# Kernel tuning notes

Measured on AMD Instinct MI355X. Metric: run time of the kernel, lower is better.

## Reference

```python
import jax, jax.numpy as jnp
import numpy as np

N_EXPERTS = 64
N_ACTIVE = 2
EPS = 1e-8


def setup_inputs() -> dict:
    key = jax.random.key(0)
    k1, k2 = jax.random.split(key)
    x = jax.random.normal(k1, (4, 4096, 2048), dtype=jnp.float32)
    # nn.Linear(dim, n_experts, bias=False) weight: (n_experts, dim)
    W_gate = jax.random.normal(k2, (N_EXPERTS, 2048), dtype=jnp.float32) * (1.0 / np.sqrt(2048))
    return {"x": x, "W_gate": W_gate}


def reference(x, W_gate):
    batch, seq_len, dim = x.shape
    x_flat = x.reshape(-1, dim)                      # (n_tokens, dim)
    n_tokens = x_flat.shape[0]

    logits = jnp.einsum('td,ed->te', x_flat, W_gate)  # (n_tokens, n_experts)
    router_probs = jax.nn.softmax(logits, axis=-1)

    top_k_weights, top_k_indices = jax.lax.top_k(router_probs, N_ACTIVE)
    top_k_weights = top_k_weights / (top_k_weights.sum(axis=-1, keepdims=True) + EPS)

    # Load-balance loss: f_i = fraction of tokens routed to expert i, P_i = mean prob
    one_hot = jax.nn.one_hot(top_k_indices, N_EXPERTS, dtype=jnp.float32)  # (t, k, e)
    tokens_per_expert = one_hot.sum(axis=(0, 1))      # (n_experts,)
    f = tokens_per_expert / (n_tokens * N_ACTIVE)
    P = router_probs.mean(axis=0)
    aux_loss = N_EXPERTS * jnp.sum(f * P)

    return top_k_indices, top_k_weights, aux_loss
```

## Files before the change

### kernel.cpp

```cpp
#include <hip/hip_runtime.h>
#include <math.h>

#define DIM   2048
#define NEXP  64
#define TPB   512
#define TOKB  64
#define KSQ   16

typedef float f32x4  __attribute__((ext_vector_type(4)));
typedef short bf16x8 __attribute__((ext_vector_type(8)));
typedef unsigned short u16;

#define MFMA __builtin_amdgcn_mfma_f32_16x16x32_bf16

__device__ __forceinline__ u16 rne_bf16(float f) {
    union { float f; unsigned u; } v; v.f = f;
    unsigned u = v.u;
    u += 0x7fffu + ((u >> 16) & 1u);
    return (u16)(u >> 16);
}
__device__ __forceinline__ float bf2f(u16 h) {
    union { unsigned u; float f; } v; v.u = ((unsigned)h) << 16;
    return v.f;
}
__device__ __forceinline__ void split3(float x, u16& a, u16& b, u16& c) {
    a = rne_bf16(x);
    float r1 = x - bf2f(a);
    b = rne_bf16(r1);
    float r2 = r1 - bf2f(b);
    c = rne_bf16(r2);
}

__device__ __forceinline__ unsigned cvt_pk(float lo, float hi) {
    unsigned r;
    asm("v_cvt_pk_bf16_f32 %0, %1, %2" : "=v"(r) : "v"(lo), "v"(hi));
    return r;
}
__device__ __forceinline__ float lof(unsigned u) {
    union { unsigned u; float f; } v; v.u = u << 16;
    return v.f;
}
__device__ __forceinline__ float hif(unsigned u) {
    union { unsigned u; float f; } v; v.u = u & 0xffff0000u;
    return v.f;
}

__device__ __forceinline__ void split3x8(f32x4 lo, f32x4 hi,
                                         bf16x8* A0, bf16x8* A1, bf16x8* A2) {
    unsigned w0[4], w1[4], w2[4];
    float e0[4] = {lo.x, lo.z, hi.x, hi.z};
    float e1[4] = {lo.y, lo.w, hi.y, hi.w};
#pragma unroll
    for (int j = 0; j < 4; ++j) {
        float a = e0[j], b = e1[j];
        unsigned p0 = cvt_pk(a, b);
        float r0 = a - lof(p0), r1 = b - hif(p0);
        unsigned p1 = cvt_pk(r0, r1);
        float s0 = r0 - lof(p1), s1 = r1 - hif(p1);
        w0[j] = p0; w1[j] = p1; w2[j] = cvt_pk(s0, s1);
    }
    *A0 = *(bf16x8*)w0;
    *A1 = *(bf16x8*)w1;
    *A2 = *(bf16x8*)w2;
}

#define GLD(GP, LP) __builtin_amdgcn_global_load_lds(                          \
        (const __attribute__((address_space(1))) unsigned*)(GP),               \
        (__attribute__((address_space(3))) unsigned*)(LP), 16, 0, 0)

__global__ __launch_bounds__(256)
void wconv(const float* __restrict__ Wg, u16* __restrict__ wp) {
    const int G  = blockIdx.x * 256 + threadIdx.x;
    const int l  = G & 63;
    const int r  = G >> 6;
    const int ks = r >> 2, et = r & 3;
    const int ex = et * 16 + (l & 15);
    const int k  = ks * 32 + (l >> 4) * 8;
    const float* src = Wg + (size_t)ex * DIM + k;
    f32x4 v0 = *(const f32x4*)src;
    f32x4 v1 = *(const f32x4*)(src + 4);
    u16 h0[8], h1[8], h2[8];
#pragma unroll
    for (int i = 0; i < 8; ++i) {
        float xv = (i < 4) ? v0[i] : v1[i - 4];
        split3(xv, h0[i], h1[i], h2[i]);
    }
    u16* dst = wp + ((size_t)(ks * 12 + et * 3)) * 512 + l * 8;
    *(bf16x8*)(dst)        = *(bf16x8*)h0;
    *(bf16x8*)(dst + 512)  = *(bf16x8*)h1;
    *(bf16x8*)(dst + 1024) = *(bf16x8*)h2;
}

__global__ __launch_bounds__(TPB, 2)
void router_main(const float* __restrict__ x, const u16* __restrict__ wp,
                 float* __restrict__ out, float* __restrict__ gCnt,
                 float* __restrict__ gPsum, int n_tokens) {
    __shared__ __align__(16) unsigned char smem[4 * 2 * 12 * 1024];
    __shared__ float cnt[NEXP];
    __shared__ float rs[TOKB];
    u16 (*bq)[2][12][512] = (u16 (*)[2][12][512])smem;
    float (*ls)[TOKB][68] = (float (*)[TOKB][68])smem;

    const int tid  = threadIdx.x;
    const int lane = tid & 63;
    const int wid  = tid >> 6;
    const int ttg  = wid & 1;
    const int kq   = wid >> 1;
    const int t0   = blockIdx.x * TOKB;

    if (tid < NEXP) cnt[tid] = 0.f;

    f32x4 acc[2][4];
#pragma unroll
    for (int t2 = 0; t2 < 2; ++t2)
#pragma unroll
        for (int et = 0; et < 4; ++et) acc[t2][et] = (f32x4){0.f, 0.f, 0.f, 0.f};

    const float* xs0 = x + (size_t)(t0 + 32 * ttg + (lane & 15)) * DIM
                         + kq * (KSQ * 32) + 8 * (lane >> 4);
    const float* xs1 = xs0 + (size_t)16 * DIM;

#define STAGEB(C) do {                                                         \
        const int g_ = kq * KSQ + (C);                                         \
        const u16* gp_ = wp + ((size_t)g_ * 12 + 6 * ttg) * 512 + lane * 8;    \
        _Pragma("unroll")                                                      \
        for (int f = 0; f < 6; ++f)                                            \
            GLD(gp_ + (size_t)f * 512, &bq[kq][(C) & 1][6 * ttg + f][0]);      \
    } while (0)

#define LOADX(S0, S1, S2, S3, C) do {                                          \
        S0 = *(const f32x4*)(xs0 + (C) * 32);                                  \
        S1 = *(const f32x4*)(xs0 + (C) * 32 + 4);                              \
        S2 = *(const f32x4*)(xs1 + (C) * 32);                                  \
        S3 = *(const f32x4*)(xs1 + (C) * 32 + 4);                              \
    } while (0)

#define ITER(C, S0, S1, S2, S3) do {                                           \
        if ((C) + 1 < KSQ) STAGEB((C) + 1);                                    \
        bf16x8 A00, A01, A02, A10, A11, A12;                                   \
        split3x8(S0, S1, &A00, &A01, &A02);                                    \
        split3x8(S2, S3, &A10, &A11, &A12);                                    \
        if ((C) + 2 < KSQ) LOADX(S0, S1, S2, S3, (C) + 2);                     \
        _Pragma("unroll")                                                      \
        for (int et = 0; et < 4; ++et) {                                       \
            bf16x8 B0 = *(const bf16x8*)&bq[kq][(C) & 1][et * 3 + 0][lane * 8];\
            bf16x8 B1 = *(const bf16x8*)&bq[kq][(C) & 1][et * 3 + 1][lane * 8];\
            bf16x8 B2 = *(const bf16x8*)&bq[kq][(C) & 1][et * 3 + 2][lane * 8];\
            acc[0][et] = MFMA(A00, B0, acc[0][et], 0, 0, 0);                   \
            acc[0][et] = MFMA(A00, B1, acc[0][et], 0, 0, 0);                   \
            acc[0][et] = MFMA(A01, B0, acc[0][et], 0, 0, 0);                   \
            acc[0][et] = MFMA(A01, B1, acc[0][et], 0, 0, 0);                   \
            acc[0][et] = MFMA(A00, B2, acc[0][et], 0, 0, 0);                   \
            acc[0][et] = MFMA(A02, B0, acc[0][et], 0, 0, 0);                   \
            acc[1][et] = MFMA(A10, B0, acc[1][et], 0, 0, 0);                   \
            acc[1][et] = MFMA(A10, B1, acc[1][et], 0, 0, 0);                   \
            acc[1][et] = MFMA(A11, B0, acc[1][et], 0, 0, 0);                   \
            acc[1][et] = MFMA(A11, B1, acc[1][et], 0, 0, 0);                   \
            acc[1][et] = MFMA(A10, B2, acc[1][et], 0, 0, 0);                   \
            acc[1][et] = MFMA(A12, B0, acc[1][et], 0, 0, 0);                   \
        }                                                                      \
        __syncthreads();                                                       \
    } while (0)

    f32x4 pa0, pa1, pa2, pa3, pb0, pb1, pb2, pb3;
    STAGEB(0);
    LOADX(pa0, pa1, pa2, pa3, 0);
    LOADX(pb0, pb1, pb2, pb3, 1);
    __syncthreads();

    for (int cc = 0; cc < KSQ; cc += 2) {
        ITER(cc,     pa0, pa1, pa2, pa3);
        ITER(cc + 1, pb0, pb1, pb2, pb3);
    }
#undef ITER
#undef LOADX
#undef STAGEB

    {
        const int e0 = lane & 15;
#pragma unroll
        for (int t2 = 0; t2 < 2; ++t2) {
            const int mr = 32 * ttg + 16 * t2 + 4 * (lane >> 4);
#pragma unroll
            for (int r = 0; r < 4; ++r) {
                ls[kq][mr + r][e0]      = acc[t2][0][r];
                ls[kq][mr + r][e0 + 16] = acc[t2][1][r];
                ls[kq][mr + r][e0 + 32] = acc[t2][2][r];
                ls[kq][mr + r][e0 + 48] = acc[t2][3][r];
            }
        }
    }
    __syncthreads();

#pragma unroll
    for (int r2 = 0; r2 < 2; ++r2) {
        const int idx = tid + TPB * r2;
        const int tk  = idx >> 4;
        const int e4  = (idx & 15) * 4;
        f32x4 v = *(const f32x4*)&ls[0][tk][e4];
        v = v + *(const f32x4*)&ls[1][tk][e4];
        v = v + *(const f32x4*)&ls[2][tk][e4];
        v = v + *(const f32x4*)&ls[3][tk][e4];
        *(f32x4*)&ls[0][tk][e4] = v;
    }
    __syncthreads();

    const int tok = tid >> 3;
    const int sub = tid & 7;
    float l8[8];
#pragma unroll
    for (int j = 0; j < 8; ++j) l8[j] = ls[0][tok][sub * 8 + j];
    float m1 = -1e30f, m2 = -1e30f;
    int   i1 = 0, i2 = 0;
#pragma unroll
    for (int j = 0; j < 8; ++j) {
        float v = l8[j]; int e = sub * 8 + j;
        if (v > m1)      { m2 = m1; i2 = i1; m1 = v; i1 = e; }
        else if (v > m2) { m2 = v; i2 = e; }
    }
#pragma unroll
    for (int off = 1; off < 8; off <<= 1) {
        float n1 = __shfl_xor(m1, off, 8); int j1 = __shfl_xor(i1, off, 8);
        float n2 = __shfl_xor(m2, off, 8); int j2 = __shfl_xor(i2, off, 8);
        bool fb = (m1 > n1) || (m1 == n1 && i1 < j1);
        float a1 = fb ? m1 : n1;  int ai = fb ? i1 : j1;
        float b1 = fb ? n1 : m1;  int bi = fb ? j1 : i1;
        float c2 = fb ? m2 : n2;  int ci = fb ? i2 : j2;
        bool bb = (b1 > c2) || (b1 == c2 && bi < ci);
        m1 = a1; i1 = ai;
        m2 = bb ? b1 : c2; i2 = bb ? bi : ci;
    }
    float psum = 0.f;
#pragma unroll
    for (int j = 0; j < 8; ++j) {
        float p = __expf(l8[j] - m1);
        psum += p;
        ls[0][tok][sub * 8 + j] = p;
    }
#pragma unroll
    for (int off = 1; off < 8; off <<= 1) psum += __shfl_xor(psum, off, 8);
    const float inv = 1.f / psum;
    if (sub == 0) {
        rs[tok] = inv;
        const float p1 = inv;
        const float p2 = __expf(m2 - m1) * inv;
        const float d  = p1 + p2 + 1e-8f;
        const int tg = t0 + tok;
        out[(size_t)tg * 2]     = (float)i1;
        out[(size_t)tg * 2 + 1] = (float)i2;
        out[(size_t)n_tokens * 2 + (size_t)tg * 2]     = p1 / d;
        out[(size_t)n_tokens * 2 + (size_t)tg * 2 + 1] = p2 / d;
        atomicAdd(&cnt[i1], 1.f);
        atomicAdd(&cnt[i2], 1.f);
    }
    __syncthreads();

    if (tid < NEXP) {
        float cs = 0.f;
#pragma unroll 8
        for (int t = 0; t < TOKB; ++t) cs += ls[0][t][tid] * rs[t];
        atomicAdd(&gPsum[tid], cs);
        atomicAdd(&gCnt[tid], cnt[tid]);
    }
}

__global__ void router_aux(const float* __restrict__ gCnt,
                           const float* __restrict__ gPsum,
                           float* __restrict__ out, int n_tokens) {
    const int e = threadIdx.x;
    float f = gCnt[e] / (float)(n_tokens * 2);
    float P = gPsum[e] / (float)n_tokens;
    float v = f * P;
#pragma unroll
    for (int o = 32; o > 0; o >>= 1) v += __shfl_down(v, o);
    if (e == 0) out[(size_t)n_tokens * 4] = 64.f * v;
}

extern "C" void kernel_launch(void* const* d_in, const int* in_sizes, int n_in,
                              void* d_out, int out_size, void* d_ws, size_t ws_size,
                              hipStream_t stream) {
    const float* x  = (const float*)d_in[0];
    const float* Wg = (const float*)d_in[1];
    float* out = (float*)d_out;
    const int n_tokens = in_sizes[0] / DIM;

    u16*   wplanes = (u16*)d_ws;
    float* gCnt    = (float*)((char*)d_ws + 256 * 3 * 512 * sizeof(u16));
    float* gPsum   = gCnt + NEXP;

    hipMemsetAsync(gCnt, 0, 2 * NEXP * sizeof(float), stream);
    hipLaunchKernelGGL(wconv, dim3(64), dim3(256), 0, stream, Wg, wplanes);
    hipLaunchKernelGGL(router_main, dim3(n_tokens / TOKB), dim3(TPB), 0, stream,
                       x, wplanes, out, gCnt, gPsum, n_tokens);
    hipLaunchKernelGGL(router_aux, dim3(1), dim3(NEXP), 0, stream,
                       gCnt, gPsum, out, n_tokens);
}
```

Before: 54.49 us.

## Give each wave private weight buffers and drop per-chunk block barriers

Re-partitions the eight waves from 2 token groups × 4 K-quarters to 2 token groups × 2 expert halves × 2 K-halves. Each wave now stages its own weight slice into a private double buffer, so the per-chunk __syncthreads is replaced by explicit vmcnt/lgkmcnt waits and sched barriers, with prefetch two chunks ahead. The x loads are now duplicated across the two expert-half waves, and the K-split reduction shrinks from four partials to two. The hand-written waitcnt counts depend on how many loads each wave issues, so a wrong count would risk reading a buffer before it has landed.

```diff
diff --git a/kernel.cpp b/kernel.cpp
--- a/kernel.cpp
+++ b/kernel.cpp
@@ -5,7 +5,7 @@
 #define NEXP  64
 #define TPB   512
 #define TOKB  64
-#define KSQ   16
+#define NKS   32
 
 typedef float f32x4  __attribute__((ext_vector_type(4)));
 typedef short bf16x8 __attribute__((ext_vector_type(8)));
@@ -95,37 +95,38 @@
 void router_main(const float* __restrict__ x, const u16* __restrict__ wp,
                  float* __restrict__ out, float* __restrict__ gCnt,
                  float* __restrict__ gPsum, int n_tokens) {
-    __shared__ __align__(16) unsigned char smem[4 * 2 * 12 * 1024];
+    __shared__ __align__(16) unsigned char smem[8 * 2 * 6 * 1024];
     __shared__ float cnt[NEXP];
     __shared__ float rs[TOKB];
-    u16 (*bq)[2][12][512] = (u16 (*)[2][12][512])smem;
+    u16 (*bq)[2][6][512] = (u16 (*)[2][6][512])smem;
     float (*ls)[TOKB][68] = (float (*)[TOKB][68])smem;
 
     const int tid  = threadIdx.x;
     const int lane = tid & 63;
     const int wid  = tid >> 6;
     const int ttg  = wid & 1;
-    const int kq   = wid >> 1;
+    const int eh   = (wid >> 1) & 1;
+    const int kh   = wid >> 2;
     const int t0   = blockIdx.x * TOKB;
 
     if (tid < NEXP) cnt[tid] = 0.f;
 
-    f32x4 acc[2][4];
+    f32x4 acc[2][2];
 #pragma unroll
     for (int t2 = 0; t2 < 2; ++t2)
 #pragma unroll
-        for (int et = 0; et < 4; ++et) acc[t2][et] = (f32x4){0.f, 0.f, 0.f, 0.f};
+        for (int e2 = 0; e2 < 2; ++e2) acc[t2][e2] = (f32x4){0.f, 0.f, 0.f, 0.f};
 
     const float* xs0 = x + (size_t)(t0 + 32 * ttg + (lane & 15)) * DIM
-                         + kq * (KSQ * 32) + 8 * (lane >> 4);
+                         + kh * (NKS * 32) + 8 * (lane >> 4);
     const float* xs1 = xs0 + (size_t)16 * DIM;
 
 #define STAGEB(C) do {                                                         \
-        const int g_ = kq * KSQ + (C);                                         \
-        const u16* gp_ = wp + ((size_t)g_ * 12 + 6 * ttg) * 512 + lane * 8;    \
+        const int g_ = kh * NKS + (C);                                         \
+        const u16* gp_ = wp + ((size_t)g_ * 12 + 6 * eh) * 512 + lane * 8;     \
         _Pragma("unroll")                                                      \
         for (int f = 0; f < 6; ++f)                                            \
-            GLD(gp_ + (size_t)f * 512, &bq[kq][(C) & 1][6 * ttg + f][0]);      \
+            GLD(gp_ + (size_t)f * 512, &bq[wid][(C) & 1][f][0]);               \
     } while (0)
 
 #define LOADX(S0, S1, S2, S3, C) do {                                          \
@@ -136,39 +137,54 @@
     } while (0)
 
 #define ITER(C, S0, S1, S2, S3) do {                                           \
-        if ((C) + 1 < KSQ) STAGEB((C) + 1);                                    \
+        if ((C) + 1 < NKS) asm volatile("s_waitcnt vmcnt(10)" ::: "memory");   \
+        else               asm volatile("s_waitcnt vmcnt(0)"  ::: "memory");   \
+        __builtin_amdgcn_sched_barrier(0);                                     \
+        bf16x8 B00 = *(const bf16x8*)&bq[wid][(C) & 1][0][lane * 8];           \
+        bf16x8 B01 = *(const bf16x8*)&bq[wid][(C) & 1][1][lane * 8];           \
+        bf16x8 B02 = *(const bf16x8*)&bq[wid][(C) & 1][2][lane * 8];           \
+        bf16x8 B10 = *(const bf16x8*)&bq[wid][(C) & 1][3][lane * 8];           \
+        bf16x8 B11 = *(const bf16x8*)&bq[wid][(C) & 1][4][lane * 8];           \
+        bf16x8 B12 = *(const bf16x8*)&bq[wid][(C) & 1][5][lane * 8];           \
         bf16x8 A00, A01, A02, A10, A11, A12;                                   \
         split3x8(S0, S1, &A00, &A01, &A02);                                    \
         split3x8(S2, S3, &A10, &A11, &A12);                                    \
-        if ((C) + 2 < KSQ) LOADX(S0, S1, S2, S3, (C) + 2);                     \
-        _Pragma("unroll")                                                      \
-        for (int et = 0; et < 4; ++et) {                                       \
-            bf16x8 B0 = *(const bf16x8*)&bq[kq][(C) & 1][et * 3 + 0][lane * 8];\
-            bf16x8 B1 = *(const bf16x8*)&bq[kq][(C) & 1][et * 3 + 1][lane * 8];\
-            bf16x8 B2 = *(const bf16x8*)&bq[kq][(C) & 1][et * 3 + 2][lane * 8];\
-            acc[0][et] = MFMA(A00, B0, acc[0][et], 0, 0, 0);                   \
-            acc[0][et] = MFMA(A00, B1, acc[0][et], 0, 0, 0);                   \
-            acc[0][et] = MFMA(A01, B0, acc[0][et], 0, 0, 0);                   \
-            acc[0][et] = MFMA(A01, B1, acc[0][et], 0, 0, 0);                   \
-            acc[0][et] = MFMA(A00, B2, acc[0][et], 0, 0, 0);                   \
-            acc[0][et] = MFMA(A02, B0, acc[0][et], 0, 0, 0);                   \
-            acc[1][et] = MFMA(A10, B0, acc[1][et], 0, 0, 0);                   \
-            acc[1][et] = MFMA(A10, B1, acc[1][et], 0, 0, 0);                   \
-            acc[1][et] = MFMA(A11, B0, acc[1][et], 0, 0, 0);                   \
-            acc[1][et] = MFMA(A11, B1, acc[1][et], 0, 0, 0);                   \
-            acc[1][et] = MFMA(A10, B2, acc[1][et], 0, 0, 0);                   \
-            acc[1][et] = MFMA(A12, B0, acc[1][et], 0, 0, 0);                   \
-        }                                                                      \
-        __syncthreads();                                                       \
+        asm volatile("s_waitcnt lgkmcnt(0)" ::: "memory");                     \
+        __builtin_amdgcn_sched_barrier(0);                                     \
+        if ((C) + 2 < NKS) { STAGEB((C) + 2); LOADX(S0, S1, S2, S3, (C) + 2); }\
+        acc[0][0] = MFMA(A00, B00, acc[0][0], 0, 0, 0);                        \
+        acc[0][0] = MFMA(A00, B01, acc[0][0], 0, 0, 0);                        \
+        acc[0][0] = MFMA(A01, B00, acc[0][0], 0, 0, 0);                        \
+        acc[0][0] = MFMA(A01, B01, acc[0][0], 0, 0, 0);                        \
+        acc[0][0] = MFMA(A00, B02, acc[0][0], 0, 0, 0);                        \
+        acc[0][0] = MFMA(A02, B00, acc[0][0], 0, 0, 0);                        \
+        acc[0][1] = MFMA(A00, B10, acc[0][1], 0, 0, 0);                        \
+        acc[0][1] = MFMA(A00, B11, acc[0][1], 0, 0, 0);                        \
+        acc[0][1] = MFMA(A01, B10, acc[0][1], 0, 0, 0);                        \
+        acc[0][1] = MFMA(A01, B11, acc[0][1], 0, 0, 0);                        \
+        acc[0][1] = MFMA(A00, B12, acc[0][1], 0, 0, 0);                        \
+        acc[0][1] = MFMA(A02, B10, acc[0][1], 0, 0, 0);                        \
+        acc[1][0] = MFMA(A10, B00, acc[1][0], 0, 0, 0);                        \
+        acc[1][0] = MFMA(A10, B01, acc[1][0], 0, 0, 0);                        \
+        acc[1][0] = MFMA(A11, B00, acc[1][0], 0, 0, 0);                        \
+        acc[1][0] = MFMA(A11, B01, acc[1][0], 0, 0, 0);                        \
+        acc[1][0] = MFMA(A10, B02, acc[1][0], 0, 0, 0);                        \
+        acc[1][0] = MFMA(A12, B00, acc[1][0], 0, 0, 0);                        \
+        acc[1][1] = MFMA(A10, B10, acc[1][1], 0, 0, 0);                        \
+        acc[1][1] = MFMA(A10, B11, acc[1][1], 0, 0, 0);                        \
+        acc[1][1] = MFMA(A11, B10, acc[1][1], 0, 0, 0);                        \
+        acc[1][1] = MFMA(A11, B11, acc[1][1], 0, 0, 0);                        \
+        acc[1][1] = MFMA(A10, B12, acc[1][1], 0, 0, 0);                        \
+        acc[1][1] = MFMA(A12, B10, acc[1][1], 0, 0, 0);                        \
     } while (0)
 
     f32x4 pa0, pa1, pa2, pa3, pb0, pb1, pb2, pb3;
     STAGEB(0);
     LOADX(pa0, pa1, pa2, pa3, 0);
+    STAGEB(1);
     LOADX(pb0, pb1, pb2, pb3, 1);
-    __syncthreads();
-
-    for (int cc = 0; cc < KSQ; cc += 2) {
+
+    for (int cc = 0; cc < NKS; cc += 2) {
         ITER(cc,     pa0, pa1, pa2, pa3);
         ITER(cc + 1, pb0, pb1, pb2, pb3);
     }
@@ -176,6 +192,8 @@
 #undef LOADX
 #undef STAGEB
 
+    __syncthreads();
+
     {
         const int e0 = lane & 15;
 #pragma unroll
@@ -183,10 +201,8 @@
             const int mr = 32 * ttg + 16 * t2 + 4 * (lane >> 4);
 #pragma unroll
             for (int r = 0; r < 4; ++r) {
-                ls[kq][mr + r][e0]      = acc[t2][0][r];
-                ls[kq][mr + r][e0 + 16] = acc[t2][1][r];
-                ls[kq][mr + r][e0 + 32] = acc[t2][2][r];
-                ls[kq][mr + r][e0 + 48] = acc[t2][3][r];
+                ls[kh][mr + r][32 * eh + e0]      = acc[t2][0][r];
+                ls[kh][mr + r][32 * eh + 16 + e0] = acc[t2][1][r];
             }
         }
     }
@@ -199,8 +215,6 @@
         const int e4  = (idx & 15) * 4;
         f32x4 v = *(const f32x4*)&ls[0][tk][e4];
         v = v + *(const f32x4*)&ls[1][tk][e4];
-        v = v + *(const f32x4*)&ls[2][tk][e4];
-        v = v + *(const f32x4*)&ls[3][tk][e4];
         *(f32x4*)&ls[0][tk][e4] = v;
     }
     __syncthreads();
```

Result: slower. 62.70 us (+15.1%).

## Use 4-wave blocks with per-wave private K slices and barrier-free pipelining

Applied to the files above, without the earlier changes.

Halves the block to 256 threads, so each wave owns one K-quarter and handles all 64 tokens (4 token tiles) instead of splitting tokens across two waves. Each wave now stages its own B fragments and synchronizes with explicit vmcnt/lgkmcnt waits and sched barriers instead of a __syncthreads per K step. This is meant to remove block-wide barrier stalls and raise MFMA density per wave. In exchange it doubles accumulator and prefetch register use and drops to one block per CU in the launch bounds, so occupancy falls. The epilogue is adapted to 4 threads per token.

```diff
diff --git a/kernel.cpp b/kernel.cpp
--- a/kernel.cpp
+++ b/kernel.cpp
@@ -3,7 +3,7 @@
 
 #define DIM   2048
 #define NEXP  64
-#define TPB   512
+#define TPB   256
 #define TOKB  64
 #define KSQ   16
 
@@ -91,7 +91,7 @@
     *(bf16x8*)(dst + 1024) = *(bf16x8*)h2;
 }
 
-__global__ __launch_bounds__(TPB, 2)
+__global__ __launch_bounds__(TPB, 1)
 void router_main(const float* __restrict__ x, const u16* __restrict__ wp,
                  float* __restrict__ out, float* __restrict__ gCnt,
                  float* __restrict__ gPsum, int n_tokens) {
@@ -103,97 +103,129 @@
 
     const int tid  = threadIdx.x;
     const int lane = tid & 63;
-    const int wid  = tid >> 6;
-    const int ttg  = wid & 1;
-    const int kq   = wid >> 1;
+    const int kq   = tid >> 6;
     const int t0   = blockIdx.x * TOKB;
 
     if (tid < NEXP) cnt[tid] = 0.f;
 
-    f32x4 acc[2][4];
-#pragma unroll
-    for (int t2 = 0; t2 < 2; ++t2)
-#pragma unroll
-        for (int et = 0; et < 4; ++et) acc[t2][et] = (f32x4){0.f, 0.f, 0.f, 0.f};
-
-    const float* xs0 = x + (size_t)(t0 + 32 * ttg + (lane & 15)) * DIM
+    f32x4 acc[4][4];
+#pragma unroll
+    for (int t = 0; t < 4; ++t)
+#pragma unroll
+        for (int e = 0; e < 4; ++e) acc[t][e] = (f32x4){0.f, 0.f, 0.f, 0.f};
+
+    const float* xt0 = x + (size_t)(t0 +  0 + (lane & 15)) * DIM
                          + kq * (KSQ * 32) + 8 * (lane >> 4);
-    const float* xs1 = xs0 + (size_t)16 * DIM;
+    const float* xt1 = xt0 + (size_t)16 * DIM;
+    const float* xt2 = xt0 + (size_t)32 * DIM;
+    const float* xt3 = xt0 + (size_t)48 * DIM;
 
 #define STAGEB(C) do {                                                         \
         const int g_ = kq * KSQ + (C);                                         \
-        const u16* gp_ = wp + ((size_t)g_ * 12 + 6 * ttg) * 512 + lane * 8;    \
+        const u16* gp_ = wp + ((size_t)g_ * 12) * 512 + lane * 8;              \
         _Pragma("unroll")                                                      \
-        for (int f = 0; f < 6; ++f)                                            \
-            GLD(gp_ + (size_t)f * 512, &bq[kq][(C) & 1][6 * ttg + f][0]);      \
+        for (int j = 0; j < 12; ++j)                                           \
+            GLD(gp_ + (size_t)j * 512, &bq[kq][(C) & 1][j][0]);                \
     } while (0)
 
-#define LOADX(S0, S1, S2, S3, C) do {                                          \
-        S0 = *(const f32x4*)(xs0 + (C) * 32);                                  \
-        S1 = *(const f32x4*)(xs0 + (C) * 32 + 4);                              \
-        S2 = *(const f32x4*)(xs1 + (C) * 32);                                  \
-        S3 = *(const f32x4*)(xs1 + (C) * 32 + 4);                              \
+#define LOADX(P0, P1, P2, P3, P4, P5, P6, P7, C) do {                          \
+        P0 = *(const f32x4*)(xt0 + (C) * 32);                                  \
+        P1 = *(const f32x4*)(xt0 + (C) * 32 + 4);                              \
+        P2 = *(const f32x4*)(xt1 + (C) * 32);                                  \
+        P3 = *(const f32x4*)(xt1 + (C) * 32 + 4);                              \
+        P4 = *(const f32x4*)(xt2 + (C) * 32);                                  \
+        P5 = *(const f32x4*)(xt2 + (C) * 32 + 4);                              \
+        P6 = *(const f32x4*)(xt3 + (C) * 32);                                  \
+        P7 = *(const f32x4*)(xt3 + (C) * 32 + 4);                              \
     } while (0)
 
-#define ITER(C, S0, S1, S2, S3) do {                                           \
-        if ((C) + 1 < KSQ) STAGEB((C) + 1);                                    \
-        bf16x8 A00, A01, A02, A10, A11, A12;                                   \
-        split3x8(S0, S1, &A00, &A01, &A02);                                    \
-        split3x8(S2, S3, &A10, &A11, &A12);                                    \
-        if ((C) + 2 < KSQ) LOADX(S0, S1, S2, S3, (C) + 2);                     \
-        _Pragma("unroll")                                                      \
-        for (int et = 0; et < 4; ++et) {                                       \
-            bf16x8 B0 = *(const bf16x8*)&bq[kq][(C) & 1][et * 3 + 0][lane * 8];\
-            bf16x8 B1 = *(const bf16x8*)&bq[kq][(C) & 1][et * 3 + 1][lane * 8];\
-            bf16x8 B2 = *(const bf16x8*)&bq[kq][(C) & 1][et * 3 + 2][lane * 8];\
-            acc[0][et] = MFMA(A00, B0, acc[0][et], 0, 0, 0);                   \
-            acc[0][et] = MFMA(A00, B1, acc[0][et], 0, 0, 0);                   \
-            acc[0][et] = MFMA(A01, B0, acc[0][et], 0, 0, 0);                   \
-            acc[0][et] = MFMA(A01, B1, acc[0][et], 0, 0, 0);                   \
-            acc[0][et] = MFMA(A00, B2, acc[0][et], 0, 0, 0);                   \
-            acc[0][et] = MFMA(A02, B0, acc[0][et], 0, 0, 0);                   \
-            acc[1][et] = MFMA(A10, B0, acc[1][et], 0, 0, 0);                   \
-            acc[1][et] = MFMA(A10, B1, acc[1][et], 0, 0, 0);                   \
-            acc[1][et] = MFMA(A11, B0, acc[1][et], 0, 0, 0);                   \
-            acc[1][et] = MFMA(A11, B1, acc[1][et], 0, 0, 0);                   \
-            acc[1][et] = MFMA(A10, B2, acc[1][et], 0, 0, 0);                   \
-            acc[1][et] = MFMA(A12, B0, acc[1][et], 0, 0, 0);                   \
+#define ETILE(E, C) do {                                                       \
+        bf16x8 B0 = *(const bf16x8*)&bq[kq][(C) & 1][(E) * 3 + 0][lane * 8];   \
+        bf16x8 B1 = *(const bf16x8*)&bq[kq][(C) & 1][(E) * 3 + 1][lane * 8];   \
+        bf16x8 B2 = *(const bf16x8*)&bq[kq][(C) & 1][(E) * 3 + 2][lane * 8];   \
+        acc[0][E] = MFMA(A00, B0, acc[0][E], 0, 0, 0);                         \
+        acc[0][E] = MFMA(A00, B1, acc[0][E], 0, 0, 0);                         \
+        acc[0][E] = MFMA(A01, B0, acc[0][E], 0, 0, 0);                         \
+        acc[0][E] = MFMA(A01, B1, acc[0][E], 0, 0, 0);                         \
+        acc[0][E] = MFMA(A00, B2, acc[0][E], 0, 0, 0);                         \
+        acc[0][E] = MFMA(A02, B0, acc[0][E], 0, 0, 0);                         \
+        acc[1][E] = MFMA(A10, B0, acc[1][E], 0, 0, 0);                         \
+        acc[1][E] = MFMA(A10, B1, acc[1][E], 0, 0, 0);                         \
+        acc[1][E] = MFMA(A11, B0, acc[1][E], 0, 0, 0);                         \
+        acc[1][E] = MFMA(A11, B1, acc[1][E], 0, 0, 0);                         \
+        acc[1][E] = MFMA(A10, B2, acc[1][E], 0, 0, 0);                         \
+        acc[1][E] = MFMA(A12, B0, acc[1][E], 0, 0, 0);                         \
+        acc[2][E] = MFMA(A20, B0, acc[2][E], 0, 0, 0);                         \
+        acc[2][E] = MFMA(A20, B1, acc[2][E], 0, 0, 0);                         \
+        acc[2][E] = MFMA(A21, B0, acc[2][E], 0, 0, 0);                         \
+        acc[2][E] = MFMA(A21, B1, acc[2][E], 0, 0, 0);                         \
+        acc[2][E] = MFMA(A20, B2, acc[2][E], 0, 0, 0);                         \
+        acc[2][E] = MFMA(A22, B0, acc[2][E], 0, 0, 0);                         \
+        acc[3][E] = MFMA(A30, B0, acc[3][E], 0, 0, 0);                         \
+        acc[3][E] = MFMA(A30, B1, acc[3][E], 0, 0, 0);                         \
+        acc[3][E] = MFMA(A31, B0, acc[3][E], 0, 0, 0);                         \
+        acc[3][E] = MFMA(A31, B1, acc[3][E], 0, 0, 0);                         \
+        acc[3][E] = MFMA(A30, B2, acc[3][E], 0, 0, 0);                         \
+        acc[3][E] = MFMA(A32, B0, acc[3][E], 0, 0, 0);                         \
+    } while (0)
+
+#define ITER(C, P0, P1, P2, P3, P4, P5, P6, P7) do {                           \
+        if ((C) + 1 < KSQ) asm volatile("s_waitcnt vmcnt(20)" ::: "memory");   \
+        else               asm volatile("s_waitcnt vmcnt(0)"  ::: "memory");   \
+        __builtin_amdgcn_sched_barrier(0);                                     \
+        bf16x8 A00, A01, A02, A10, A11, A12, A20, A21, A22, A30, A31, A32;     \
+        split3x8(P0, P1, &A00, &A01, &A02);                                    \
+        split3x8(P2, P3, &A10, &A11, &A12);                                    \
+        split3x8(P4, P5, &A20, &A21, &A22);                                    \
+        split3x8(P6, P7, &A30, &A31, &A32);                                    \
+        ETILE(0, C);                                                           \
+        ETILE(1, C);                                                           \
+        ETILE(2, C);                                                           \
+        ETILE(3, C);                                                           \
+        asm volatile("s_waitcnt lgkmcnt(0)" ::: "memory");                     \
+        __builtin_amdgcn_sched_barrier(0);                                     \
+        if ((C) + 2 < KSQ) {                                                   \
+            STAGEB((C) + 2);                                                   \
+            LOADX(P0, P1, P2, P3, P4, P5, P6, P7, (C) + 2);                    \
         }                                                                      \
-        __syncthreads();                                                       \
     } while (0)
 
-    f32x4 pa0, pa1, pa2, pa3, pb0, pb1, pb2, pb3;
+    f32x4 pa0, pa1, pa2, pa3, pa4, pa5, pa6, pa7;
+    f32x4 pb0, pb1, pb2, pb3, pb4, pb5, pb6, pb7;
     STAGEB(0);
-    LOADX(pa0, pa1, pa2, pa3, 0);
-    LOADX(pb0, pb1, pb2, pb3, 1);
-    __syncthreads();
+    LOADX(pa0, pa1, pa2, pa3, pa4, pa5, pa6, pa7, 0);
+    STAGEB(1);
+    LOADX(pb0, pb1, pb2, pb3, pb4, pb5, pb6, pb7, 1);
 
     for (int cc = 0; cc < KSQ; cc += 2) {
-        ITER(cc,     pa0, pa1, pa2, pa3);
-        ITER(cc + 1, pb0, pb1, pb2, pb3);
+        ITER(cc,     pa0, pa1, pa2, pa3, pa4, pa5, pa6, pa7);
+        ITER(cc + 1, pb0, pb1, pb2, pb3, pb4, pb5, pb6, pb7);
     }
 #undef ITER
+#undef ETILE
 #undef LOADX
 #undef STAGEB
 
+    __syncthreads();
+
     {
         const int e0 = lane & 15;
 #pragma unroll
-        for (int t2 = 0; t2 < 2; ++t2) {
-            const int mr = 32 * ttg + 16 * t2 + 4 * (lane >> 4);
+        for (int t = 0; t < 4; ++t) {
+            const int mr = 16 * t + 4 * (lane >> 4);
 #pragma unroll
             for (int r = 0; r < 4; ++r) {
-                ls[kq][mr + r][e0]      = acc[t2][0][r];
-                ls[kq][mr + r][e0 + 16] = acc[t2][1][r];
-                ls[kq][mr + r][e0 + 32] = acc[t2][2][r];
-                ls[kq][mr + r][e0 + 48] = acc[t2][3][r];
+                ls[kq][mr + r][e0]      = acc[t][0][r];
+                ls[kq][mr + r][e0 + 16] = acc[t][1][r];
+                ls[kq][mr + r][e0 + 32] = acc[t][2][r];
+                ls[kq][mr + r][e0 + 48] = acc[t][3][r];
             }
         }
     }
     __syncthreads();
 
 #pragma unroll
-    for (int r2 = 0; r2 < 2; ++r2) {
+    for (int r2 = 0; r2 < 4; ++r2) {
         const int idx = tid + TPB * r2;
         const int tk  = idx >> 4;
         const int e4  = (idx & 15) * 4;
@@ -205,23 +237,23 @@
     }
     __syncthreads();
 
-    const int tok = tid >> 3;
-    const int sub = tid & 7;
-    float l8[8];
-#pragma unroll
-    for (int j = 0; j < 8; ++j) l8[j] = ls[0][tok][sub * 8 + j];
+    const int tok = tid >> 2;
+    const int sub = tid & 3;
+    float l16[16];
+#pragma unroll
+    for (int j = 0; j < 16; ++j) l16[j] = ls[0][tok][sub * 16 + j];
     float m1 = -1e30f, m2 = -1e30f;
     int   i1 = 0, i2 = 0;
 #pragma unroll
-    for (int j = 0; j < 8; ++j) {
-        float v = l8[j]; int e = sub * 8 + j;
+    for (int j = 0; j < 16; ++j) {
+        float v = l16[j]; int e = sub * 16 + j;
         if (v > m1)      { m2 = m1; i2 = i1; m1 = v; i1 = e; }
         else if (v > m2) { m2 = v; i2 = e; }
     }
 #pragma unroll
-    for (int off = 1; off < 8; off <<= 1) {
-        float n1 = __shfl_xor(m1, off, 8); int j1 = __shfl_xor(i1, off, 8);
-        float n2 = __shfl_xor(m2, off, 8); int j2 = __shfl_xor(i2, off, 8);
+    for (int off = 1; off < 4; off <<= 1) {
+        float n1 = __shfl_xor(m1, off, 4); int j1 = __shfl_xor(i1, off, 4);
+        float n2 = __shfl_xor(m2, off, 4); int j2 = __shfl_xor(i2, off, 4);
         bool fb = (m1 > n1) || (m1 == n1 && i1 < j1);
         float a1 = fb ? m1 : n1;  int ai = fb ? i1 : j1;
         float b1 = fb ? n1 : m1;  int bi = fb ? j1 : i1;
@@ -232,13 +264,13 @@
     }
     float psum = 0.f;
 #pragma unroll
-    for (int j = 0; j < 8; ++j) {
-        float p = __expf(l8[j] - m1);
-        psum += p;
-        ls[0][tok][sub * 8 + j] = p;
-    }
-#pragma unroll
-    for (int off = 1; off < 8; off <<= 1) psum += __shfl_xor(psum, off, 8);
+    for (int j = 0; j < 16; ++j) {
+        float pv = __expf(l16[j] - m1);
+        psum += pv;
+        ls[0][tok][sub * 16 + j] = pv;
+    }
+#pragma unroll
+    for (int off = 1; off < 4; off <<= 1) psum += __shfl_xor(psum, off, 4);
     const float inv = 1.f / psum;
     if (sub == 0) {
         rs[tok] = inv;
```

New measurement: 50.46 us. 7.4% less time.
